# Performance work log

Hardware: AMD Instinct MI355X
Metric: run time of the kernel (lower is better)

## Reference

```python
import jax, jax.numpy as jnp
import numpy as np

EPS = 1e-9
C, Hd, Wd = 3, 64, 64  # input_dimensions[1:]

def setup_inputs() -> dict:
    key = jax.random.key(0)
    ks = jax.random.split(key, 8)
    S, B = 8, 512
    num_digits, num_style, num_hidden, bott, num_pixels = 10, 50, 512, 160, C * Hd * Wd
    return {
        "digits": jax.random.uniform(ks[0], (S, B, num_digits), dtype=jnp.float32),
        "styles": jax.random.normal(ks[1], (S, B, num_style), dtype=jnp.float32),
        "images": jax.random.uniform(ks[2], (S, B, C, Hd, Wd), dtype=jnp.float32),
        "W_h": jax.random.normal(ks[3], (num_digits + num_style, num_hidden), dtype=jnp.float32) * 0.05,
        "b_h": jnp.zeros((num_hidden,), jnp.float32),
        "W1": jax.random.normal(ks[4], (num_hidden, bott), dtype=jnp.float32) * 0.05,
        "b1": jnp.zeros((bott,), jnp.float32),
        "W2": jax.random.normal(ks[5], (bott, num_pixels), dtype=jnp.float32) * 0.05,
        "b2": jnp.zeros((num_pixels,), jnp.float32),
    }

def reference(digits, styles, images, W_h, b_h, W1, b1, W2, b2):
    # dec_hidden: Linear + ReLU, fully batched over [S, B]
    h = jax.nn.relu(jnp.concatenate([digits, styles], axis=-1) @ W_h + b_h)  # [S,B,Hn]
    # hidden_pass (original loops per-sample; here a single batched GEMM chain)
    t = jax.nn.selu(h @ W1 + b1)                 # [S,B,160]
    x_hat = jax.nn.sigmoid(t @ W2 + b2)          # [S,B,P]
    S, B, _ = x_hat.shape
    images_mean = x_hat.reshape(S, B, C, Hd, Wd)
    # eps-guarded BCE-style log-likelihood loss, summed over last dim only
    loss = -(jnp.log(images_mean + EPS) * images
             + jnp.log(1.0 - images_mean + EPS) * (1.0 - images)).sum(-1)  # [S,B,C,Hd]
    return loss
```

## Files before the change

kernel.cpp:

```cpp
#include <hip/hip_runtime.h>
#include <hip/hip_bf16.h>
#include <math.h>


#define SELU_SCALE 1.0507009873554804934193349852946f
#define SELU_ALPHA 1.6732632423543772848170429916717f

typedef __attribute__((ext_vector_type(8))) short bf16x8;
typedef __attribute__((ext_vector_type(4))) float f32x4;

static __device__ __forceinline__ short f2bf(float x) {
    __hip_bfloat16 h = __float2bfloat16(x);
    short s;
    __builtin_memcpy(&s, &h, 2);
    return s;
}

__global__ __launch_bounds__(256) void w2_pack_kernel(
    const float* __restrict__ W2,
    __hip_bfloat16* __restrict__ w2f)
{
    __shared__ float tile[32][64];
    const int colBase = blockIdx.x * 64;
    const int kkBase  = blockIdx.y * 32;
    const int tid = threadIdx.x;

    for (int i = tid; i < 32 * 64; i += 256)
        tile[i >> 6][i & 63] = W2[(size_t)(kkBase + (i >> 6)) * 12288 + colBase + (i & 63)];
    __syncthreads();

    const int c16 = tid >> 6;
    const int lane = tid & 63;
    const int lr = lane & 15, lh = lane >> 4;

    bf16x8 v;
#pragma unroll
    for (int j = 0; j < 8; ++j)
        v[j] = f2bf(tile[lh * 8 + j][c16 * 16 + lr]);

    const size_t chunk = (size_t)(blockIdx.x * 4 + c16) * 5 + blockIdx.y;
    *(bf16x8*)((short*)w2f + chunk * 512 + lane * 8) = v;
}

__global__ __launch_bounds__(512) void dec_hidden_kernel(
    const float* __restrict__ digits,
    const float* __restrict__ styles,
    const float* __restrict__ Wh,
    const float* __restrict__ bh,
    __hip_bfloat16* __restrict__ h)
{
    __shared__ float cat_s[8][60];
    const int tid = threadIdx.x;
    const int rowBase = blockIdx.x * 8;

    for (int i = tid; i < 8 * 60; i += 512) {
        const int r = i / 60, k = i % 60;
        const int row = rowBase + r;
        cat_s[r][k] = (k < 10) ? digits[row * 10 + k]
                               : styles[row * 50 + (k - 10)];
    }
    __syncthreads();

    float acc[8];
    const float bias = bh[tid];
#pragma unroll
    for (int r = 0; r < 8; ++r) acc[r] = bias;

    for (int k = 0; k < 60; ++k) {
        const float w = Wh[k * 512 + tid];
#pragma unroll
        for (int r = 0; r < 8; ++r) acc[r] = fmaf(cat_s[r][k], w, acc[r]);
    }
#pragma unroll
    for (int r = 0; r < 8; ++r)
        h[(size_t)(rowBase + r) * 512 + tid] = __float2bfloat16(fmaxf(acc[r], 0.0f));
}

__global__ __launch_bounds__(192) void hidden1_kernel(
    const __hip_bfloat16* __restrict__ h,
    const float* __restrict__ W1,
    const float* __restrict__ b1,
    __hip_bfloat16* __restrict__ t)
{
    __shared__ float h_s[4 * 512];
    const int tid = threadIdx.x;
    const int rowBase = blockIdx.x * 4;
    const __hip_bfloat16* hsrc = h + (size_t)rowBase * 512;
    for (int i = tid; i < 4 * 512; i += 192) h_s[i] = __bfloat162float(hsrc[i]);
    __syncthreads();

    if (tid < 160) {
        float acc[4];
        const float bias = b1[tid];
#pragma unroll
        for (int r = 0; r < 4; ++r) acc[r] = bias;

        for (int k = 0; k < 512; k += 4) {
            const float w0 = W1[(size_t)(k + 0) * 160 + tid];
            const float w1 = W1[(size_t)(k + 1) * 160 + tid];
            const float w2 = W1[(size_t)(k + 2) * 160 + tid];
            const float w3 = W1[(size_t)(k + 3) * 160 + tid];
#pragma unroll
            for (int r = 0; r < 4; ++r) {
                const float4 hv = *(const float4*)&h_s[r * 512 + k];
                float a = acc[r];
                a = fmaf(hv.x, w0, a);
                a = fmaf(hv.y, w1, a);
                a = fmaf(hv.z, w2, a);
                a = fmaf(hv.w, w3, a);
                acc[r] = a;
            }
        }
#pragma unroll
        for (int r = 0; r < 4; ++r) {
            const float z = acc[r];
            const float s = (z > 0.0f) ? (SELU_SCALE * z)
                                       : (SELU_SCALE * SELU_ALPHA * expm1f(z));
            t[(size_t)(rowBase + r) * 160 + tid] = __float2bfloat16(s);
        }
    }
}

__global__ __launch_bounds__(256) void t_pack_kernel(
    const __hip_bfloat16* __restrict__ t,
    __hip_bfloat16* __restrict__ tf)
{
    const int lane = threadIdx.x & 63;
    const int cidx = blockIdx.x * 4 + (threadIdx.x >> 6);
    const int r16 = cidx / 5, kk = cidx % 5;
    const short* tb = (const short*)t;
    const bf16x8 v = *(const bf16x8*)(tb
        + (size_t)(r16 * 16 + (lane & 15)) * 160 + kk * 32 + (lane >> 4) * 8);
    *(bf16x8*)((short*)tf + (size_t)cidx * 512 + lane * 8) = v;
}

__global__ __launch_bounds__(256, 4) void out_loss_mfma_kernel(
    const __hip_bfloat16* __restrict__ tf,
    const __hip_bfloat16* __restrict__ w2f,
    const float* __restrict__ b2,
    const float* __restrict__ images,
    float* __restrict__ out)
{
    __shared__ float ims[4][2048];

    const int tid = threadIdx.x;
    const int lane = tid & 63;
    const int wv = tid >> 6;
    const int rowBase = blockIdx.y * 128 + wv * 32;
    const int colBase = blockIdx.x * 64;
    const int lr = lane & 15;
    const int lh = lane >> 4;

    const short* wfb = (const short*)w2f;
    const short* tfb = (const short*)tf;
    const char* imb = (const char*)images;

    {
        const int rsub = lane >> 4;
        const int m = lane & 15;
#pragma unroll
        for (int w = 0; w < 8; ++w) {
            const int r = w * 4 + rsub;
            const size_t gb = (size_t)(rowBase + r) * 49152 + (size_t)colBase * 4
                            + (size_t)((16 * m) ^ ((r & 15) << 4));
            __builtin_amdgcn_global_load_lds((const uint32_t*)(imb + gb),
                (uint32_t*)&ims[wv][w * 256], 16, 0, 0);
        }
    }

    const int c16base = blockIdx.x * 4;
    const int r16base = rowBase >> 4;

    f32x4 acc[4][2] = {};
#pragma unroll
    for (int kk = 0; kk < 5; ++kk) {
        bf16x8 bT[2], aW[4];
#pragma unroll
        for (int r = 0; r < 2; ++r)
            bT[r] = *(const bf16x8*)(tfb
                + ((size_t)(r16base + r) * 5 + kk) * 512 + lane * 8);
#pragma unroll
        for (int c = 0; c < 4; ++c)
            aW[c] = *(const bf16x8*)(wfb
                + ((size_t)(c16base + c) * 5 + kk) * 512 + lane * 8);
#pragma unroll
        for (int c = 0; c < 4; ++c)
#pragma unroll
            for (int r = 0; r < 2; ++r)
                acc[c][r] = __builtin_amdgcn_mfma_f32_16x16x32_bf16(
                    aW[c], bT[r], acc[c][r], 0, 0, 0);
    }

    float4 bc[4];
#pragma unroll
    for (int c = 0; c < 4; ++c)
        bc[c] = *(const float4*)(b2 + colBase + c * 16 + lh * 4);

    asm volatile("s_waitcnt vmcnt(0)" ::: "memory");
    __builtin_amdgcn_sched_barrier(0);

    const float* myq = ims[wv];
#pragma unroll
    for (int rw = 0; rw < 2; ++rw) {
        float mx = 0.f;
        float pr = 1.f;
        float zi = 0.f;
#pragma unroll
        for (int c = 0; c < 4; ++c) {
            const int fidx = (rw * 16 + lr) * 64 + ((lh * 4 + c * 16) ^ (lr << 2));
            const float4 im4 = *(const float4*)&myq[fidx];
            const float imv[4] = {im4.x, im4.y, im4.z, im4.w};
            const float bcv[4] = {bc[c].x, bc[c].y, bc[c].z, bc[c].w};
#pragma unroll
            for (int j = 0; j < 4; ++j) {
                const float z = acc[c][rw][j] + bcv[j];
                mx += fmaxf(z, 0.0f);
                pr *= 1.0f + __expf(-fabsf(z));
                zi = fmaf(z, imv[j], zi);
            }
        }
        float part = mx + __logf(pr) - zi;

        part += __shfl_xor(part, 16);
        part += __shfl_xor(part, 32);

        if (lane < 16)
            out[(size_t)(rowBase + rw * 16 + lane) * 192 + blockIdx.x] = part;
    }
}

extern "C" void kernel_launch(void* const* d_in, const int* in_sizes, int n_in,
                              void* d_out, int out_size, void* d_ws, size_t ws_size,
                              hipStream_t stream) {
    const float* digits = (const float*)d_in[0];
    const float* styles = (const float*)d_in[1];
    const float* images = (const float*)d_in[2];
    const float* Wh     = (const float*)d_in[3];
    const float* bh     = (const float*)d_in[4];
    const float* W1     = (const float*)d_in[5];
    const float* b1     = (const float*)d_in[6];
    const float* W2     = (const float*)d_in[7];
    const float* b2     = (const float*)d_in[8];
    float* out = (float*)d_out;

    const int R = 4096;

    __hip_bfloat16* h   = (__hip_bfloat16*)d_ws;
    __hip_bfloat16* tt  = h + (size_t)R * 512;
    __hip_bfloat16* w2f = tt + (size_t)R * 160;
    __hip_bfloat16* tf  = w2f + (size_t)12288 * 160;

    dim3 gridP(192, 5);
    w2_pack_kernel<<<gridP, 256, 0, stream>>>(W2, w2f);

    dec_hidden_kernel<<<R / 8, 512, 0, stream>>>(digits, styles, Wh, bh, h);
    hidden1_kernel<<<R / 4, 192, 0, stream>>>(h, W1, b1, tt);
    t_pack_kernel<<<320, 256, 0, stream>>>(tt, tf);

    dim3 grid3(192, 32);
    out_loss_mfma_kernel<<<grid3, 256, 0, stream>>>(tf, w2f, b2, images, out);
}
```

Measured before the change: 93.72 us.

## Load images directly into registers, swap grid order, and double hidden1 rows per block

```diff
diff --git a/kernel.cpp b/kernel.cpp
--- a/kernel.cpp
+++ b/kernel.cpp
@@ -82,18 +82,18 @@
     const float* __restrict__ b1,
     __hip_bfloat16* __restrict__ t)
 {
-    __shared__ float h_s[4 * 512];
-    const int tid = threadIdx.x;
-    const int rowBase = blockIdx.x * 4;
+    __shared__ float h_s[8 * 512];
+    const int tid = threadIdx.x;
+    const int rowBase = blockIdx.x * 8;
     const __hip_bfloat16* hsrc = h + (size_t)rowBase * 512;
-    for (int i = tid; i < 4 * 512; i += 192) h_s[i] = __bfloat162float(hsrc[i]);
+    for (int i = tid; i < 8 * 512; i += 192) h_s[i] = __bfloat162float(hsrc[i]);
     __syncthreads();
 
     if (tid < 160) {
-        float acc[4];
+        float acc[8];
         const float bias = b1[tid];
 #pragma unroll
-        for (int r = 0; r < 4; ++r) acc[r] = bias;
+        for (int r = 0; r < 8; ++r) acc[r] = bias;
 
         for (int k = 0; k < 512; k += 4) {
             const float w0 = W1[(size_t)(k + 0) * 160 + tid];
@@ -101,7 +101,7 @@
             const float w2 = W1[(size_t)(k + 2) * 160 + tid];
             const float w3 = W1[(size_t)(k + 3) * 160 + tid];
 #pragma unroll
-            for (int r = 0; r < 4; ++r) {
+            for (int r = 0; r < 8; ++r) {
                 const float4 hv = *(const float4*)&h_s[r * 512 + k];
                 float a = acc[r];
                 a = fmaf(hv.x, w0, a);
@@ -112,7 +112,7 @@
             }
         }
 #pragma unroll
-        for (int r = 0; r < 4; ++r) {
+        for (int r = 0; r < 8; ++r) {
             const float z = acc[r];
             const float s = (z > 0.0f) ? (SELU_SCALE * z)
                                        : (SELU_SCALE * SELU_ALPHA * expm1f(z));
@@ -141,34 +141,29 @@
     const float* __restrict__ images,
     float* __restrict__ out)
 {
-    __shared__ float ims[4][2048];
-
     const int tid = threadIdx.x;
     const int lane = tid & 63;
     const int wv = tid >> 6;
-    const int rowBase = blockIdx.y * 128 + wv * 32;
-    const int colBase = blockIdx.x * 64;
+    const int rowBase = blockIdx.x * 128 + wv * 32;
+    const int colBase = blockIdx.y * 64;
     const int lr = lane & 15;
     const int lh = lane >> 4;
 
+    float4 img[2][4];
+    {
+        const float* imgB = images + colBase + lh * 4;
+#pragma unroll
+        for (int rw = 0; rw < 2; ++rw)
+#pragma unroll
+            for (int c = 0; c < 4; ++c)
+                img[rw][c] = *(const float4*)(imgB
+                    + (size_t)(rowBase + rw * 16 + lr) * 12288 + c * 16);
+    }
+    __builtin_amdgcn_sched_barrier(0);
+
     const short* wfb = (const short*)w2f;
     const short* tfb = (const short*)tf;
-    const char* imb = (const char*)images;
-
-    {
-        const int rsub = lane >> 4;
-        const int m = lane & 15;
-#pragma unroll
-        for (int w = 0; w < 8; ++w) {
-            const int r = w * 4 + rsub;
-            const size_t gb = (size_t)(rowBase + r) * 49152 + (size_t)colBase * 4
-                            + (size_t)((16 * m) ^ ((r & 15) << 4));
-            __builtin_amdgcn_global_load_lds((const uint32_t*)(imb + gb),
-                (uint32_t*)&ims[wv][w * 256], 16, 0, 0);
-        }
-    }
-
-    const int c16base = blockIdx.x * 4;
+    const int c16base = blockIdx.y * 4;
     const int r16base = rowBase >> 4;
 
     f32x4 acc[4][2] = {};
@@ -196,10 +191,6 @@
     for (int c = 0; c < 4; ++c)
         bc[c] = *(const float4*)(b2 + colBase + c * 16 + lh * 4);
 
-    asm volatile("s_waitcnt vmcnt(0)" ::: "memory");
-    __builtin_amdgcn_sched_barrier(0);
-
-    const float* myq = ims[wv];
 #pragma unroll
     for (int rw = 0; rw < 2; ++rw) {
         float mx = 0.f;
@@ -207,9 +198,8 @@
         float zi = 0.f;
 #pragma unroll
         for (int c = 0; c < 4; ++c) {
-            const int fidx = (rw * 16 + lr) * 64 + ((lh * 4 + c * 16) ^ (lr << 2));
-            const float4 im4 = *(const float4*)&myq[fidx];
-            const float imv[4] = {im4.x, im4.y, im4.z, im4.w};
+            const float imv[4] = {img[rw][c].x, img[rw][c].y,
+                                  img[rw][c].z, img[rw][c].w};
             const float bcv[4] = {bc[c].x, bc[c].y, bc[c].z, bc[c].w};
 #pragma unroll
             for (int j = 0; j < 4; ++j) {
@@ -225,7 +215,7 @@
         part += __shfl_xor(part, 32);
 
         if (lane < 16)
-            out[(size_t)(rowBase + rw * 16 + lane) * 192 + blockIdx.x] = part;
+            out[(size_t)(rowBase + rw * 16 + lane) * 192 + blockIdx.y] = part;
     }
 }
 
@@ -254,9 +244,9 @@
     w2_pack_kernel<<<gridP, 256, 0, stream>>>(W2, w2f);
 
     dec_hidden_kernel<<<R / 8, 512, 0, stream>>>(digits, styles, Wh, bh, h);
-    hidden1_kernel<<<R / 4, 192, 0, stream>>>(h, W1, b1, tt);
+    hidden1_kernel<<<R / 8, 192, 0, stream>>>(h, W1, b1, tt);
     t_pack_kernel<<<320, 256, 0, stream>>>(tt, tf);
 
-    dim3 grid3(192, 32);
+    dim3 grid3(32, 192);
     out_loss_mfma_kernel<<<grid3, 256, 0, stream>>>(tf, w2f, b2, images, out);
 }
```

New measurement: 112.3 us. 1.2x slower.

## Fuse hidden layer, bottleneck layer and t packing into one kernel

Applied to the files above, without the earlier changes.

```diff
diff --git a/kernel.cpp b/kernel.cpp
--- a/kernel.cpp
+++ b/kernel.cpp
@@ -42,18 +42,23 @@
     *(bf16x8*)((short*)w2f + chunk * 512 + lane * 8) = v;
 }
 
-__global__ __launch_bounds__(512) void dec_hidden_kernel(
+__global__ __launch_bounds__(512) void dec_fused_kernel(
     const float* __restrict__ digits,
     const float* __restrict__ styles,
     const float* __restrict__ Wh,
     const float* __restrict__ bh,
-    __hip_bfloat16* __restrict__ h)
+    const float* __restrict__ W1,
+    const float* __restrict__ b1,
+    __hip_bfloat16* __restrict__ tf)
 {
-    __shared__ float cat_s[8][60];
+    __shared__ float cat_s[16][60];
+    __shared__ float h_s[16 * 512];
+    __shared__ float t_s[16][161];
+
     const int tid = threadIdx.x;
-    const int rowBase = blockIdx.x * 8;
-
-    for (int i = tid; i < 8 * 60; i += 512) {
+    const int rowBase = blockIdx.x * 16;
+
+    for (int i = tid; i < 16 * 60; i += 512) {
         const int r = i / 60, k = i % 60;
         const int row = rowBase + r;
         cat_s[r][k] = (k < 10) ? digits[row * 10 + k]
@@ -61,48 +66,39 @@
     }
     __syncthreads();
 
-    float acc[8];
-    const float bias = bh[tid];
-#pragma unroll
-    for (int r = 0; r < 8; ++r) acc[r] = bias;
-
-    for (int k = 0; k < 60; ++k) {
-        const float w = Wh[k * 512 + tid];
-#pragma unroll
-        for (int r = 0; r < 8; ++r) acc[r] = fmaf(cat_s[r][k], w, acc[r]);
-    }
-#pragma unroll
-    for (int r = 0; r < 8; ++r)
-        h[(size_t)(rowBase + r) * 512 + tid] = __float2bfloat16(fmaxf(acc[r], 0.0f));
-}
-
-__global__ __launch_bounds__(192) void hidden1_kernel(
-    const __hip_bfloat16* __restrict__ h,
-    const float* __restrict__ W1,
-    const float* __restrict__ b1,
-    __hip_bfloat16* __restrict__ t)
-{
-    __shared__ float h_s[4 * 512];
-    const int tid = threadIdx.x;
-    const int rowBase = blockIdx.x * 4;
-    const __hip_bfloat16* hsrc = h + (size_t)rowBase * 512;
-    for (int i = tid; i < 4 * 512; i += 192) h_s[i] = __bfloat162float(hsrc[i]);
-    __syncthreads();
-
-    if (tid < 160) {
-        float acc[4];
-        const float bias = b1[tid];
-#pragma unroll
-        for (int r = 0; r < 4; ++r) acc[r] = bias;
+    {
+        float acc[16];
+        const float bias = bh[tid];
+#pragma unroll
+        for (int r = 0; r < 16; ++r) acc[r] = bias;
+        for (int k = 0; k < 60; ++k) {
+            const float w = Wh[k * 512 + tid];
+#pragma unroll
+            for (int r = 0; r < 16; ++r) acc[r] = fmaf(cat_s[r][k], w, acc[r]);
+        }
+#pragma unroll
+        for (int r = 0; r < 16; ++r)
+            h_s[r * 512 + tid] = fmaxf(acc[r], 0.0f);
+    }
+    __syncthreads();
+
+    if (tid < 320) {
+        const int rh = (tid >= 160) ? 1 : 0;
+        const int col = tid - rh * 160;
+        const int r0 = rh * 8;
+        float acc[8];
+        const float bias = b1[col];
+#pragma unroll
+        for (int r = 0; r < 8; ++r) acc[r] = bias;
 
         for (int k = 0; k < 512; k += 4) {
-            const float w0 = W1[(size_t)(k + 0) * 160 + tid];
-            const float w1 = W1[(size_t)(k + 1) * 160 + tid];
-            const float w2 = W1[(size_t)(k + 2) * 160 + tid];
-            const float w3 = W1[(size_t)(k + 3) * 160 + tid];
-#pragma unroll
-            for (int r = 0; r < 4; ++r) {
-                const float4 hv = *(const float4*)&h_s[r * 512 + k];
+            const float w0 = W1[(size_t)(k + 0) * 160 + col];
+            const float w1 = W1[(size_t)(k + 1) * 160 + col];
+            const float w2 = W1[(size_t)(k + 2) * 160 + col];
+            const float w3 = W1[(size_t)(k + 3) * 160 + col];
+#pragma unroll
+            for (int r = 0; r < 8; ++r) {
+                const float4 hv = *(const float4*)&h_s[(r0 + r) * 512 + k];
                 float a = acc[r];
                 a = fmaf(hv.x, w0, a);
                 a = fmaf(hv.y, w1, a);
@@ -112,29 +108,28 @@
             }
         }
 #pragma unroll
-        for (int r = 0; r < 4; ++r) {
+        for (int r = 0; r < 8; ++r) {
             const float z = acc[r];
             const float s = (z > 0.0f) ? (SELU_SCALE * z)
                                        : (SELU_SCALE * SELU_ALPHA * expm1f(z));
-            t[(size_t)(rowBase + r) * 160 + tid] = __float2bfloat16(s);
-        }
-    }
-}
-
-__global__ __launch_bounds__(256) void t_pack_kernel(
-    const __hip_bfloat16* __restrict__ t,
-    __hip_bfloat16* __restrict__ tf)
-{
-    const int lane = threadIdx.x & 63;
-    const int cidx = blockIdx.x * 4 + (threadIdx.x >> 6);
-    const int r16 = cidx / 5, kk = cidx % 5;
-    const short* tb = (const short*)t;
-    const bf16x8 v = *(const bf16x8*)(tb
-        + (size_t)(r16 * 16 + (lane & 15)) * 160 + kk * 32 + (lane >> 4) * 8);
-    *(bf16x8*)((short*)tf + (size_t)cidx * 512 + lane * 8) = v;
-}
-
-__global__ __launch_bounds__(256, 4) void out_loss_mfma_kernel(
+            t_s[r0 + r][col] = s;
+        }
+    }
+    __syncthreads();
+
+    if (tid < 320) {
+        const int kk = tid >> 6;
+        const int l = tid & 63;
+        const int lr = l & 15, lh = l >> 4;
+        bf16x8 v;
+#pragma unroll
+        for (int j = 0; j < 8; ++j)
+            v[j] = f2bf(t_s[lr][kk * 32 + lh * 8 + j]);
+        *(bf16x8*)((short*)tf + ((size_t)blockIdx.x * 5 + kk) * 512 + l * 8) = v;
+    }
+}
+
+__global__ __launch_bounds__(256, 5) void out_loss_mfma_kernel(
     const __hip_bfloat16* __restrict__ tf,
     const __hip_bfloat16* __restrict__ w2f,
     const float* __restrict__ b2,
@@ -243,19 +238,13 @@
     const float* b2     = (const float*)d_in[8];
     float* out = (float*)d_out;
 
-    const int R = 4096;
-
-    __hip_bfloat16* h   = (__hip_bfloat16*)d_ws;
-    __hip_bfloat16* tt  = h + (size_t)R * 512;
-    __hip_bfloat16* w2f = tt + (size_t)R * 160;
+    __hip_bfloat16* w2f = (__hip_bfloat16*)d_ws;
     __hip_bfloat16* tf  = w2f + (size_t)12288 * 160;
 
     dim3 gridP(192, 5);
     w2_pack_kernel<<<gridP, 256, 0, stream>>>(W2, w2f);
 
-    dec_hidden_kernel<<<R / 8, 512, 0, stream>>>(digits, styles, Wh, bh, h);
-    hidden1_kernel<<<R / 4, 192, 0, stream>>>(h, W1, b1, tt);
-    t_pack_kernel<<<320, 256, 0, stream>>>(tt, tf);
+    dec_fused_kernel<<<256, 512, 0, stream>>>(digits, styles, Wh, bh, W1, b1, tf);
 
     dim3 grid3(192, 32);
     out_loss_mfma_kernel<<<grid3, 256, 0, stream>>>(tf, w2f, b2, images, out);
```

New measurement: 91.46 us. 2.4% less time.
